# Performance work log

Hardware: AMD Instinct MI355X
Metric: run time of the kernel (lower is better)

## Reference

```python
import jax, jax.numpy as jnp
import numpy as np

B, S, H, D = 4, 8192, 8, 64  # batch, seq, heads, head_dim
M = 64                        # num random features
EPS = 1e-6


def setup_inputs() -> dict:
    key = jax.random.key(0)
    k1, k2, k3, k4 = jax.random.split(key, 4)
    qs = jax.random.normal(k1, (B, S, H, D), dtype=jnp.float32)
    ks = jax.random.normal(k2, (B, S, H, D), dtype=jnp.float32)
    vs = jax.random.normal(k3, (B, S, H, D), dtype=jnp.float32)
    proj = jax.random.normal(k4, (M, D), dtype=jnp.float32)
    return {"qs": qs, "ks": ks, "vs": vs, "proj": proj}


def _phi(x, proj):
    # stable positive softmax kernel: exp(x @ proj^T - ||x||^2/2) / sqrt(m)
    m = proj.shape[0]
    x_proj = jnp.einsum('...d,md->...m', x, proj)
    h = jnp.sum(jnp.square(x), axis=-1, keepdims=True) * 0.5
    return jnp.exp(x_proj - h) / jnp.sqrt(jnp.asarray(m, x.dtype))


def reference(qs, ks, vs, proj):
    Bq, Q, Hh, Dqk = qs.shape
    K = ks.shape[1]
    Dv = vs.shape[-1]
    # (B, S, H, D) -> (B*H, S, D)
    q = qs.transpose(0, 2, 1, 3).reshape(-1, Q, Dqk)
    k = ks.transpose(0, 2, 1, 3).reshape(-1, K, Dqk)
    v = vs.transpose(0, 2, 1, 3).reshape(-1, K, Dv)
    normalizer = 1.0 / jnp.power(jnp.asarray(Dqk, q.dtype), 0.25)
    q_prime = _phi(q * normalizer, proj)  # (B*H, Q, M)
    k_prime = _phi(k * normalizer, proj)  # (B*H, K, M)
    # fast_attend: linear-time attention
    c = jnp.concatenate([v, jnp.ones((*v.shape[:-1], 1), v.dtype)], axis=-1)  # (B*H, K, Dv+1)
    buf1 = jnp.einsum('bkm,bkc->bmc', k_prime, c)   # (B*H, M, Dv+1)
    buf2 = jnp.einsum('bqm,bmc->bqc', q_prime, buf1)  # (B*H, Q, Dv+1)
    num, den = buf2[..., :-1], buf2[..., -1]
    den = jnp.where(den < EPS, EPS, den)
    ctx = num / den[..., None]
    return ctx.reshape(Bq, Hh, Q, Dv).transpose(0, 2, 1, 3)
```

## Files before the change

### kernel.cpp

```cpp
#include <hip/hip_runtime.h>
#include <hip/hip_bf16.h>

#define S_ 8192
#define H_ 8
#define D_ 64
#define M_ 64
#define BH_ 32
#define CPK_ 80
#define NCH_ 16
#define NCHQ 16
#define TILE 64
#define QTILES (S_ / NCHQ / TILE)

typedef short bf16x8 __attribute__((ext_vector_type(8)));
typedef float f32x4 __attribute__((ext_vector_type(4)));

constexpr float XS_ = 0.35355339059327373f * 1.4426950408889634f;
constexpr float HS_ = 0.34657359027997264f;
constexpr float EPS_ = 1e-6f;

__device__ __forceinline__ unsigned short f2bf(float f) {
    unsigned int u = __float_as_uint(f);
    u += 0x7FFFu + ((u >> 16) & 1u);
    return (unsigned short)(u >> 16);
}
__device__ __forceinline__ unsigned int pkbf(float lo, float hi) {
    __hip_bfloat162 t = __float22bfloat162_rn(float2{lo, hi});
    return *reinterpret_cast<unsigned int*>(&t);
}
__device__ __forceinline__ float fexp2(float x) { return __builtin_amdgcn_exp2f(x); }

#define MFMA(a, b, c) __builtin_amdgcn_mfma_f32_16x16x32_bf16((a), (b), (c), 0, 0, 0)
#define SWZ(byteoff, row) ((byteoff) ^ (((row) & 7) << 4))

__global__ void __launch_bounds__(256, 2)
fa_k(const float* __restrict__ ks, const float* __restrict__ vs,
     const float* __restrict__ proj, float* __restrict__ partial)
{
    const int chunk = blockIdx.x;
    const int bh    = blockIdx.y;
    const int b = bh >> 3, h = bh & 7;
    const int tid = threadIdx.x, wid = tid >> 6, lane = tid & 63;
    const int l15 = lane & 15, g = lane >> 4;

    __shared__ __align__(16) char vT[4][2][64 * 64];
    __shared__ float red[M_ * CPK_];

    const size_t rs = (size_t)H_ * D_;
    const float* kb = ks + ((size_t)b * S_ * H_ + h) * D_;
    const float* vb = vs + ((size_t)b * S_ * H_ + h) * D_;
    const int rbase = chunk * 512 + wid * 128;

    bf16x8 pf[4][2];
#pragma unroll
    for (int mt = 0; mt < 4; ++mt)
#pragma unroll
        for (int kk = 0; kk < 2; ++kk) {
            const float* p = proj + (mt * 16 + l15) * D_ + kk * 32 + g * 8;
            float4 a = *(const float4*)p, c = *(const float4*)(p + 4);
            union { bf16x8 v; unsigned int u[4]; } F;
            F.u[0] = pkbf(a.x, a.y); F.u[1] = pkbf(a.z, a.w);
            F.u[2] = pkbf(c.x, c.y); F.u[3] = pkbf(c.z, c.w);
            pf[mt][kk] = F.v;
        }

    bf16x8 onef = {0, 0, 0, 0, 0, 0, 0, 0};
    if (l15 == 0) {
#pragma unroll
        for (int j = 0; j < 8; ++j) onef[j] = (short)0x3F80;
    }

    f32x4 acc[4][5];
#pragma unroll
    for (int mt = 0; mt < 4; ++mt)
#pragma unroll
        for (int ci = 0; ci < 5; ++ci) acc[mt][ci] = (f32x4){0.f, 0.f, 0.f, 0.f};

    f32x4 paE[4];
    float hrE[4];

    auto loadX = [&](int t, float4* kp, float4* vp) {
        const float* kr = kb + (size_t)(rbase + t * 16 + l15) * rs;
        kp[0] = *(const float4*)(kr + g * 8);
        kp[1] = *(const float4*)(kr + g * 8 + 4);
        kp[2] = *(const float4*)(kr + 32 + g * 8);
        kp[3] = *(const float4*)(kr + 32 + g * 8 + 4);
        const float* vr = vb + (size_t)(rbase + t * 16 + l15) * rs;
        vp[0] = *(const float4*)(vr + g * 8);
        vp[1] = *(const float4*)(vr + g * 8 + 4);
        vp[2] = *(const float4*)(vr + 32 + g * 8);
        vp[3] = *(const float4*)(vr + 32 + g * 8 + 4);
    };

    auto body = [&](int t, const float4* kc, const float4* vc,
                    float4* kn2, float4* vn2) {
        if (t + 2 < 8) loadX(t + 2, kn2, vn2);

        float kx[16];
#pragma unroll
        for (int i = 0; i < 4; ++i) {
            kx[4*i+0] = kc[i].x * XS_; kx[4*i+1] = kc[i].y * XS_;
            kx[4*i+2] = kc[i].z * XS_; kx[4*i+3] = kc[i].w * XS_;
        }
        float sq = 0.f;
#pragma unroll
        for (int j = 0; j < 16; ++j) sq += kx[j] * kx[j];
        sq += __shfl_xor(sq, 16);
        sq += __shfl_xor(sq, 32);
        float hrow = sq * HS_ + 3.0f;

        union { bf16x8 v; unsigned int u[4]; } A0, A1;
#pragma unroll
        for (int i = 0; i < 4; ++i) {
            A0.u[i] = pkbf(kx[2*i], kx[2*i+1]);
            A1.u[i] = pkbf(kx[8+2*i], kx[9+2*i]);
        }

        f32x4 pa[4];
#pragma unroll
        for (int mt = 0; mt < 4; ++mt) {
            pa[mt] = (f32x4){0.f, 0.f, 0.f, 0.f};
            pa[mt] = MFMA(A0.v, pf[mt][0], pa[mt]);
            pa[mt] = MFMA(A1.v, pf[mt][1], pa[mt]);
        }

        float hr[4];
#pragma unroll
        for (int r = 0; r < 4; ++r) hr[r] = __shfl(hrow, 4 * g + r);

        {
            char* vtp = (char*)vT + wid * 8192 + ((t >> 1) & 1) * 4096;
            int slot2 = 2 * (((l15 >> 2) & 3) * 8 + 4 * (t & 1) + (l15 & 3));
            float vv[16];
#pragma unroll
            for (int i = 0; i < 4; ++i) {
                vv[4*i+0] = vc[i].x; vv[4*i+1] = vc[i].y;
                vv[4*i+2] = vc[i].z; vv[4*i+3] = vc[i].w;
            }
#pragma unroll
            for (int p2 = 0; p2 < 4; ++p2) {
                int cA = g * 8 + 2 * p2;
                unsigned int pA = pkbf(vv[2*p2], vv[2*p2+1]);
                *(unsigned short*)(vtp + cA * 64 + (slot2 ^ ((cA & 3) << 4))) =
                    (unsigned short)pA;
                int cB = cA + 1;
                *(unsigned short*)(vtp + cB * 64 + (slot2 ^ ((cB & 3) << 4))) =
                    (unsigned short)(pA >> 16);
                int cC = 32 + cA;
                unsigned int pB = pkbf(vv[8+2*p2], vv[9+2*p2]);
                *(unsigned short*)(vtp + cC * 64 + (slot2 ^ ((cC & 3) << 4))) =
                    (unsigned short)pB;
                int cD = cC + 1;
                *(unsigned short*)(vtp + cD * 64 + (slot2 ^ ((cD & 3) << 4))) =
                    (unsigned short)(pB >> 16);
            }
        }

        if ((t & 1) == 0) {
#pragma unroll
            for (int mt = 0; mt < 4; ++mt) paE[mt] = pa[mt];
#pragma unroll
            for (int r = 0; r < 4; ++r) hrE[r] = hr[r];
        } else {
            bf16x8 eA[4];
#pragma unroll
            for (int mt = 0; mt < 4; ++mt) {
                union { bf16x8 v; unsigned int u[4]; } E;
                E.u[0] = pkbf(fexp2(paE[mt][0]-hrE[0]), fexp2(paE[mt][1]-hrE[1]));
                E.u[1] = pkbf(fexp2(paE[mt][2]-hrE[2]), fexp2(paE[mt][3]-hrE[3]));
                E.u[2] = pkbf(fexp2(pa[mt][0]-hr[0]),   fexp2(pa[mt][1]-hr[1]));
                E.u[3] = pkbf(fexp2(pa[mt][2]-hr[2]),   fexp2(pa[mt][3]-hr[3]));
                eA[mt] = E.v;
            }
            const char* vb2 = (const char*)vT + wid * 8192 + ((t >> 1) & 1) * 4096;
            bf16x8 vB[4];
#pragma unroll
            for (int ct = 0; ct < 4; ++ct) {
                int c = ct * 16 + l15;
                vB[ct] = *(const bf16x8*)(vb2 + c * 64 + ((16 * g) ^ ((c & 3) << 4)));
            }
#pragma unroll
            for (int mt = 0; mt < 4; ++mt) {
#pragma unroll
                for (int ct = 0; ct < 4; ++ct)
                    acc[mt][ct] = MFMA(eA[mt], vB[ct], acc[mt][ct]);
                acc[mt][4] = MFMA(eA[mt], onef, acc[mt][4]);
            }
        }
    };

    float4 kA[4], vA[4], kB[4], vB_[4], kC[4], vC[4];
    loadX(0, kA, vA);
    loadX(1, kB, vB_);
    body(0, kA, vA, kC, vC);
    body(1, kB, vB_, kA, vA);
    body(2, kC, vC, kB, vB_);
    body(3, kA, vA, kC, vC);
    body(4, kB, vB_, kA, vA);
    body(5, kC, vC, kB, vB_);
    body(6, kA, vA, kC, vC);
    body(7, kB, vB_, kA, vA);

    for (int i = tid; i < M_ * CPK_; i += 256) red[i] = 0.f;
    __syncthreads();
    for (int w = 0; w < 4; ++w) {
        if (wid == w) {
#pragma unroll
            for (int mt = 0; mt < 4; ++mt)
#pragma unroll
                for (int ct = 0; ct < 5; ++ct)
#pragma unroll
                    for (int r = 0; r < 4; ++r)
                        red[(mt*16 + 4*g + r) * CPK_ + ct*16 + l15] += acc[mt][ct][r];
        }
        __syncthreads();
    }
    float* dst = partial + ((size_t)bh * NCH_ + chunk) * (M_ * CPK_);
    for (int i = tid; i < M_ * CPK_; i += 256) dst[i] = red[i];
}

__global__ void __launch_bounds__(256)
fa_r(const float* __restrict__ partial, float* __restrict__ buf1, int nch)
{
    int e = blockIdx.x * 256 + threadIdx.x;
    if (e >= BH_ * M_ * CPK_) return;
    int bh = e / (M_ * CPK_);
    int r  = e - bh * (M_ * CPK_);
    const float* src = partial + (size_t)bh * nch * (M_ * CPK_) + r;
    float s0 = 0.f, s1 = 0.f, s2 = 0.f, s3 = 0.f;
    int ch = 0;
    for (; ch + 4 <= nch; ch += 4) {
        s0 += src[(size_t)(ch + 0) * (M_ * CPK_)];
        s1 += src[(size_t)(ch + 1) * (M_ * CPK_)];
        s2 += src[(size_t)(ch + 2) * (M_ * CPK_)];
        s3 += src[(size_t)(ch + 3) * (M_ * CPK_)];
    }
    for (; ch < nch; ++ch) s0 += src[(size_t)ch * (M_ * CPK_)];
    buf1[e] = (s0 + s1) + (s2 + s3);
}

__global__ void __launch_bounds__(256)
fa_q(const float* __restrict__ qs, const float* __restrict__ proj,
     const float* __restrict__ buf1, float* __restrict__ out)
{
    const int chunk = blockIdx.x;
    const int bh    = blockIdx.y;
    const int b = bh >> 3, h = bh & 7;
    const int tid = threadIdx.x, wid = tid >> 6, lane = tid & 63;
    const int l15 = lane & 15, g = lane >> 4;

    __shared__ __align__(16) char eLb[2][TILE * M_ * 2];
    __shared__ __align__(16) char b1tb[CPK_ * M_ * 2];

    const int rows = S_ / NCHQ;
    const int s0 = chunk * rows;
    const size_t rs = (size_t)H_ * D_;
    const float* qb = qs + ((size_t)b * S_ * H_ + h) * D_;

    const float* b1 = buf1 + (size_t)bh * (M_ * CPK_);
    for (int i = tid; i < M_ * CPK_; i += 256) {
        int m = i / CPK_, c = i - m * CPK_;
        *(unsigned short*)(b1tb + SWZ(c * 128 + 2 * m, c)) = f2bf(b1[i]);
    }

    bf16x8 pf[4][2];
#pragma unroll
    for (int mt = 0; mt < 4; ++mt)
#pragma unroll
        for (int kk = 0; kk < 2; ++kk) {
            const float* p = proj + (mt * 16 + l15) * D_ + kk * 32 + g * 8;
            float4 a = *(const float4*)p, c = *(const float4*)(p + 4);
            union { bf16x8 v; unsigned int u[4]; } F;
            F.u[0] = pkbf(a.x, a.y); F.u[1] = pkbf(a.z, a.w);
            F.u[2] = pkbf(c.x, c.y); F.u[3] = pkbf(c.z, c.w);
            pf[mt][kk] = F.v;
        }
    __syncthreads();

    bf16x8 af3[5][2];
#pragma unroll
    for (int ci = 0; ci < 5; ++ci)
#pragma unroll
        for (int kk = 0; kk < 2; ++kk) {
            int c = ci * 16 + l15;
            af3[ci][kk] = *(const bf16x8*)(b1tb + SWZ(c * 128 + 16 * g + 64 * kk, c));
        }

    auto loadQ = [&](int t, float4* qp) {
        int sb = s0 + t * TILE;
        const float* qrow = qb + (size_t)(sb + wid * 16 + l15) * rs;
        qp[0] = *(const float4*)(qrow + g * 8);
        qp[1] = *(const float4*)(qrow + g * 8 + 4);
        qp[2] = *(const float4*)(qrow + 32 + g * 8);
        qp[3] = *(const float4*)(qrow + 32 + g * 8 + 4);
    };

    auto body = [&](int t, int p, const float4* qc, float4* qn) {
        if (t + 1 < QTILES) loadQ(t + 1, qn);

        float kx[16];
#pragma unroll
        for (int i = 0; i < 4; ++i) {
            kx[4 * i + 0] = qc[i].x * XS_; kx[4 * i + 1] = qc[i].y * XS_;
            kx[4 * i + 2] = qc[i].z * XS_; kx[4 * i + 3] = qc[i].w * XS_;
        }
        float sq = 0.f;
#pragma unroll
        for (int j = 0; j < 16; ++j) sq += kx[j] * kx[j];
        sq += __shfl_xor(sq, 16);
        sq += __shfl_xor(sq, 32);
        float hrow = sq * HS_ + 3.0f;

        union { bf16x8 v; unsigned int u[4]; } A0, A1;
#pragma unroll
        for (int i = 0; i < 4; ++i) {
            A0.u[i] = pkbf(kx[2 * i], kx[2 * i + 1]);
            A1.u[i] = pkbf(kx[8 + 2 * i], kx[9 + 2 * i]);
        }

        f32x4 pa[4];
#pragma unroll
        for (int mt = 0; mt < 4; ++mt) {
            pa[mt] = (f32x4){0.f, 0.f, 0.f, 0.f};
            pa[mt] = MFMA(A0.v, pf[mt][0], pa[mt]);
            pa[mt] = MFMA(A1.v, pf[mt][1], pa[mt]);
        }

        float hr[4];
#pragma unroll
        for (int r = 0; r < 4; ++r) hr[r] = __shfl(hrow, 4 * g + r);

        char* elp = eLb[p];
#pragma unroll
        for (int mt = 0; mt < 4; ++mt) {
            int m = mt * 16 + l15;
            float e0 = fexp2(pa[mt][0] - hr[0]);
            float e1 = fexp2(pa[mt][1] - hr[1]);
            float e2 = fexp2(pa[mt][2] - hr[2]);
            float e3 = fexp2(pa[mt][3] - hr[3]);
            unsigned int p01 = pkbf(e0, e1), p23 = pkbf(e2, e3);
            int q0 = wid * 16 + 4 * g;
            *(unsigned short*)(elp + SWZ((q0 + 0) * 128 + 2 * m, q0 + 0)) =
                (unsigned short)p01;
            *(unsigned short*)(elp + SWZ((q0 + 1) * 128 + 2 * m, q0 + 1)) =
                (unsigned short)(p01 >> 16);
            *(unsigned short*)(elp + SWZ((q0 + 2) * 128 + 2 * m, q0 + 2)) =
                (unsigned short)p23;
            *(unsigned short*)(elp + SWZ((q0 + 3) * 128 + 2 * m, q0 + 3)) =
                (unsigned short)(p23 >> 16);
        }
        __syncthreads();

        bf16x8 b3[2];
        {
            int qrow = wid * 16 + l15;
            b3[0] = *(const bf16x8*)(elp + SWZ(qrow * 128 + 16 * g, qrow));
            b3[1] = *(const bf16x8*)(elp + SWZ(qrow * 128 + 16 * g + 64, qrow));
        }
        f32x4 dt[5];
#pragma unroll
        for (int ci = 0; ci < 5; ++ci) {
            dt[ci] = (f32x4){0.f, 0.f, 0.f, 0.f};
            dt[ci] = MFMA(af3[ci][0], b3[0], dt[ci]);
            dt[ci] = MFMA(af3[ci][1], b3[1], dt[ci]);
        }

        float den = __shfl(dt[4][0], l15);
        float rd = 1.0f / fmaxf(den, EPS_);

        int sg = s0 + t * TILE + wid * 16 + l15;
        size_t base = (((size_t)b * S_ + sg) * H_ + h) * D_;
#pragma unroll
        for (int ci = 0; ci < 4; ++ci) {
            f32x4 o;
#pragma unroll
            for (int r = 0; r < 4; ++r) o[r] = dt[ci][r] * rd;
            *(f32x4*)(out + base + ci * 16 + 4 * g) = o;
        }
    };

    float4 qa[4], qb2[4];
    loadQ(0, qa);
    for (int t = 0; t < QTILES; t += 2) {
        body(t, 0, qa, qb2);
        body(t + 1, 1, qb2, qa);
    }
}

extern "C" void kernel_launch(void* const* d_in, const int* in_sizes, int n_in,
                              void* d_out, int out_size, void* d_ws, size_t ws_size,
                              hipStream_t stream)
{
    const float* qs   = (const float*)d_in[0];
    const float* ks   = (const float*)d_in[1];
    const float* vs   = (const float*)d_in[2];
    const float* proj = (const float*)d_in[3];
    float* out = (float*)d_out;

    float* partial = (float*)d_ws;
    float* buf1 = partial + (size_t)BH_ * NCH_ * (M_ * CPK_);

    fa_k<<<dim3(NCH_, BH_), 256, 0, stream>>>(ks, vs, proj, partial);
    int nred = (BH_ * M_ * CPK_ + 255) / 256;
    fa_r<<<dim3(nred), 256, 0, stream>>>(partial, buf1, NCH_);
    fa_q<<<dim3(NCHQ, BH_), 256, 0, stream>>>(qs, proj, buf1, out);
}
```

Baseline: 74.15 us.

## Stream K/V tiles into LDS with async global_load_lds and smaller blocks

The K-feature kernel now loads K and V rows straight into a four-deep LDS ring with global_load_lds, paced by explicit vmcnt waits. This replaces the register prefetch and the manual bf16 transpose scatter of V into LDS. V is read back from the raw fp32 layout and packed to bf16 at MFMA time. Blocks shrink to two waves, the chunk count doubles to keep the grid filled, and the reduction kernel sums twice as many partials. The gain in load overlap comes with more partial traffic and more reduction work in the second kernel.

```diff
diff --git a/kernel.cpp b/kernel.cpp
--- a/kernel.cpp
+++ b/kernel.cpp
@@ -7,7 +7,7 @@
 #define M_ 64
 #define BH_ 32
 #define CPK_ 80
-#define NCH_ 16
+#define NCHK 32
 #define NCHQ 16
 #define TILE 64
 #define QTILES (S_ / NCHQ / TILE)
@@ -33,23 +33,26 @@
 #define MFMA(a, b, c) __builtin_amdgcn_mfma_f32_16x16x32_bf16((a), (b), (c), 0, 0, 0)
 #define SWZ(byteoff, row) ((byteoff) ^ (((row) & 7) << 4))
 
-__global__ void __launch_bounds__(256, 2)
+#define GLDS(src, dst) __builtin_amdgcn_global_load_lds( \
+    (const __attribute__((address_space(1))) void*)(src), \
+    (__attribute__((address_space(3))) void*)(dst), 16, 0, 0)
+
+__global__ void __launch_bounds__(128)
 fa_k(const float* __restrict__ ks, const float* __restrict__ vs,
      const float* __restrict__ proj, float* __restrict__ partial)
 {
+    __shared__ __align__(16) char pool[2][4][8192];
+
     const int chunk = blockIdx.x;
     const int bh    = blockIdx.y;
     const int b = bh >> 3, h = bh & 7;
     const int tid = threadIdx.x, wid = tid >> 6, lane = tid & 63;
     const int l15 = lane & 15, g = lane >> 4;
 
-    __shared__ __align__(16) char vT[4][2][64 * 64];
-    __shared__ float red[M_ * CPK_];
-
     const size_t rs = (size_t)H_ * D_;
     const float* kb = ks + ((size_t)b * S_ * H_ + h) * D_;
     const float* vb = vs + ((size_t)b * S_ * H_ + h) * D_;
-    const int rbase = chunk * 512 + wid * 128;
+    const int rbase = chunk * 256 + wid * 128;
 
     bf16x8 pf[4][2];
 #pragma unroll
@@ -76,31 +79,35 @@
 #pragma unroll
         for (int ci = 0; ci < 5; ++ci) acc[mt][ci] = (f32x4){0.f, 0.f, 0.f, 0.f};
 
-    f32x4 paE[4];
-    float hrE[4];
-
-    auto loadX = [&](int t, float4* kp, float4* vp) {
-        const float* kr = kb + (size_t)(rbase + t * 16 + l15) * rs;
-        kp[0] = *(const float4*)(kr + g * 8);
-        kp[1] = *(const float4*)(kr + g * 8 + 4);
-        kp[2] = *(const float4*)(kr + 32 + g * 8);
-        kp[3] = *(const float4*)(kr + 32 + g * 8 + 4);
-        const float* vr = vb + (size_t)(rbase + t * 16 + l15) * rs;
-        vp[0] = *(const float4*)(vr + g * 8);
-        vp[1] = *(const float4*)(vr + g * 8 + 4);
-        vp[2] = *(const float4*)(vr + 32 + g * 8);
-        vp[3] = *(const float4*)(vr + 32 + g * 8 + 4);
-    };
-
-    auto body = [&](int t, const float4* kc, const float4* vc,
-                    float4* kn2, float4* vn2) {
-        if (t + 2 < 8) loadX(t + 2, kn2, vn2);
-
+    auto stage = [&](int t) {
+        char* kd = pool[wid][t & 3];
+        char* vd = kd + 4096;
+        const float* krow = kb + (size_t)(rbase + t * 16 + l15) * rs;
+        const float* vrow = vb + (size_t)(rbase + t * 16 + l15) * rs;
+#pragma unroll
+        for (int i = 0; i < 4; ++i) {
+            int c0 = (i >> 1) * 32 + (i & 1) * 4 + 8 * g;
+            GLDS(krow + c0, kd + i * 1024);
+            GLDS(vrow + c0, vd + i * 1024);
+        }
+    };
+
+    f32x4 paE[4], paO[4];
+    float hrE[4], hrO[4];
+
+    auto consumeP = [&](int t, f32x4* pa, float* hr) {
+        const char* kd = pool[wid][t & 3];
+        f32x4 r0 = *(const f32x4*)(kd + lane * 16);
+        f32x4 r1 = *(const f32x4*)(kd + 1024 + lane * 16);
+        f32x4 r2 = *(const f32x4*)(kd + 2048 + lane * 16);
+        f32x4 r3 = *(const f32x4*)(kd + 3072 + lane * 16);
         float kx[16];
 #pragma unroll
-        for (int i = 0; i < 4; ++i) {
-            kx[4*i+0] = kc[i].x * XS_; kx[4*i+1] = kc[i].y * XS_;
-            kx[4*i+2] = kc[i].z * XS_; kx[4*i+3] = kc[i].w * XS_;
+        for (int j = 0; j < 4; ++j) {
+            kx[j]      = r0[j] * XS_;
+            kx[4 + j]  = r1[j] * XS_;
+            kx[8 + j]  = r2[j] * XS_;
+            kx[12 + j] = r3[j] * XS_;
         }
         float sq = 0.f;
 #pragma unroll
@@ -112,98 +119,80 @@
         union { bf16x8 v; unsigned int u[4]; } A0, A1;
 #pragma unroll
         for (int i = 0; i < 4; ++i) {
-            A0.u[i] = pkbf(kx[2*i], kx[2*i+1]);
-            A1.u[i] = pkbf(kx[8+2*i], kx[9+2*i]);
-        }
-
-        f32x4 pa[4];
+            A0.u[i] = pkbf(kx[2 * i], kx[2 * i + 1]);
+            A1.u[i] = pkbf(kx[8 + 2 * i], kx[9 + 2 * i]);
+        }
 #pragma unroll
         for (int mt = 0; mt < 4; ++mt) {
             pa[mt] = (f32x4){0.f, 0.f, 0.f, 0.f};
             pa[mt] = MFMA(A0.v, pf[mt][0], pa[mt]);
             pa[mt] = MFMA(A1.v, pf[mt][1], pa[mt]);
         }
-
-        float hr[4];
 #pragma unroll
         for (int r = 0; r < 4; ++r) hr[r] = __shfl(hrow, 4 * g + r);
-
-        {
-            char* vtp = (char*)vT + wid * 8192 + ((t >> 1) & 1) * 4096;
-            int slot2 = 2 * (((l15 >> 2) & 3) * 8 + 4 * (t & 1) + (l15 & 3));
-            float vv[16];
-#pragma unroll
-            for (int i = 0; i < 4; ++i) {
-                vv[4*i+0] = vc[i].x; vv[4*i+1] = vc[i].y;
-                vv[4*i+2] = vc[i].z; vv[4*i+3] = vc[i].w;
-            }
-#pragma unroll
-            for (int p2 = 0; p2 < 4; ++p2) {
-                int cA = g * 8 + 2 * p2;
-                unsigned int pA = pkbf(vv[2*p2], vv[2*p2+1]);
-                *(unsigned short*)(vtp + cA * 64 + (slot2 ^ ((cA & 3) << 4))) =
-                    (unsigned short)pA;
-                int cB = cA + 1;
-                *(unsigned short*)(vtp + cB * 64 + (slot2 ^ ((cB & 3) << 4))) =
-                    (unsigned short)(pA >> 16);
-                int cC = 32 + cA;
-                unsigned int pB = pkbf(vv[8+2*p2], vv[9+2*p2]);
-                *(unsigned short*)(vtp + cC * 64 + (slot2 ^ ((cC & 3) << 4))) =
-                    (unsigned short)pB;
-                int cD = cC + 1;
-                *(unsigned short*)(vtp + cD * 64 + (slot2 ^ ((cD & 3) << 4))) =
-                    (unsigned short)(pB >> 16);
-            }
-        }
-
-        if ((t & 1) == 0) {
-#pragma unroll
-            for (int mt = 0; mt < 4; ++mt) paE[mt] = pa[mt];
-#pragma unroll
-            for (int r = 0; r < 4; ++r) hrE[r] = hr[r];
-        } else {
-            bf16x8 eA[4];
-#pragma unroll
-            for (int mt = 0; mt < 4; ++mt) {
-                union { bf16x8 v; unsigned int u[4]; } E;
-                E.u[0] = pkbf(fexp2(paE[mt][0]-hrE[0]), fexp2(paE[mt][1]-hrE[1]));
-                E.u[1] = pkbf(fexp2(paE[mt][2]-hrE[2]), fexp2(paE[mt][3]-hrE[3]));
-                E.u[2] = pkbf(fexp2(pa[mt][0]-hr[0]),   fexp2(pa[mt][1]-hr[1]));
-                E.u[3] = pkbf(fexp2(pa[mt][2]-hr[2]),   fexp2(pa[mt][3]-hr[3]));
-                eA[mt] = E.v;
-            }
-            const char* vb2 = (const char*)vT + wid * 8192 + ((t >> 1) & 1) * 4096;
-            bf16x8 vB[4];
-#pragma unroll
-            for (int ct = 0; ct < 4; ++ct) {
-                int c = ct * 16 + l15;
-                vB[ct] = *(const bf16x8*)(vb2 + c * 64 + ((16 * g) ^ ((c & 3) << 4)));
-            }
-#pragma unroll
-            for (int mt = 0; mt < 4; ++mt) {
-#pragma unroll
-                for (int ct = 0; ct < 4; ++ct)
-                    acc[mt][ct] = MFMA(eA[mt], vB[ct], acc[mt][ct]);
-                acc[mt][4] = MFMA(eA[mt], onef, acc[mt][4]);
-            }
-        }
-    };
-
-    float4 kA[4], vA[4], kB[4], vB_[4], kC[4], vC[4];
-    loadX(0, kA, vA);
-    loadX(1, kB, vB_);
-    body(0, kA, vA, kC, vC);
-    body(1, kB, vB_, kA, vA);
-    body(2, kC, vC, kB, vB_);
-    body(3, kA, vA, kC, vC);
-    body(4, kB, vB_, kA, vA);
-    body(5, kC, vC, kB, vB_);
-    body(6, kA, vA, kC, vC);
-    body(7, kB, vB_, kA, vA);
-
-    for (int i = tid; i < M_ * CPK_; i += 256) red[i] = 0.f;
+    };
+
+    auto EV = [&](int t) {
+        const char* vE = pool[wid][t & 3] + 4096;
+        const char* vO = pool[wid][(t + 1) & 3] + 4096;
+        bf16x8 eA[4];
+#pragma unroll
+        for (int mt = 0; mt < 4; ++mt) {
+            union { bf16x8 v; unsigned int u[4]; } E;
+            E.u[0] = pkbf(fexp2(paE[mt][0] - hrE[0]), fexp2(paE[mt][1] - hrE[1]));
+            E.u[1] = pkbf(fexp2(paE[mt][2] - hrE[2]), fexp2(paE[mt][3] - hrE[3]));
+            E.u[2] = pkbf(fexp2(paO[mt][0] - hrO[0]), fexp2(paO[mt][1] - hrO[1]));
+            E.u[3] = pkbf(fexp2(paO[mt][2] - hrO[2]), fexp2(paO[mt][3] - hrO[3]));
+            eA[mt] = E.v;
+        }
+#pragma unroll
+        for (int ct = 0; ct < 4; ++ct) {
+            int c = ct * 16 + l15;
+            int ic = ((c >> 5) << 1) | ((c >> 2) & 1);
+            int boff = ic * 1024 + ((c & 31) >> 3) * 256 + (c & 3) * 4 + 64 * g;
+            float e0 = *(const float*)(vE + boff);
+            float e1 = *(const float*)(vE + boff + 16);
+            float e2 = *(const float*)(vE + boff + 32);
+            float e3 = *(const float*)(vE + boff + 48);
+            float o0 = *(const float*)(vO + boff);
+            float o1 = *(const float*)(vO + boff + 16);
+            float o2 = *(const float*)(vO + boff + 32);
+            float o3 = *(const float*)(vO + boff + 48);
+            union { bf16x8 v; unsigned int u[4]; } B;
+            B.u[0] = pkbf(e0, e1); B.u[1] = pkbf(e2, e3);
+            B.u[2] = pkbf(o0, o1); B.u[3] = pkbf(o2, o3);
+#pragma unroll
+            for (int mt = 0; mt < 4; ++mt)
+                acc[mt][ct] = MFMA(eA[mt], B.v, acc[mt][ct]);
+        }
+#pragma unroll
+        for (int mt = 0; mt < 4; ++mt)
+            acc[mt][4] = MFMA(eA[mt], onef, acc[mt][4]);
+    };
+
+    stage(0); stage(1); stage(2); stage(3);
+
+#define PAIR(T, W1, W2, DOSTAGE)                                   \
+    asm volatile("s_waitcnt vmcnt(" #W1 ")" ::: "memory");         \
+    __builtin_amdgcn_sched_barrier(0);                             \
+    consumeP(T, paE, hrE);                                         \
+    asm volatile("s_waitcnt vmcnt(" #W2 ")" ::: "memory");         \
+    __builtin_amdgcn_sched_barrier(0);                             \
+    consumeP(T + 1, paO, hrO);                                     \
+    EV(T);                                                         \
+    if (DOSTAGE) { stage(T + 4); stage(T + 5); }
+
+    PAIR(0, 24, 16, 1)
+    PAIR(2, 24, 16, 1)
+    PAIR(4, 24, 16, 0)
+    PAIR(6, 8, 0, 0)
+#undef PAIR
+
     __syncthreads();
-    for (int w = 0; w < 4; ++w) {
+    float* red = (float*)pool;
+    for (int i = tid; i < M_ * CPK_; i += 128) red[i] = 0.f;
+    __syncthreads();
+    for (int w = 0; w < 2; ++w) {
         if (wid == w) {
 #pragma unroll
             for (int mt = 0; mt < 4; ++mt)
@@ -211,12 +200,13 @@
                 for (int ct = 0; ct < 5; ++ct)
 #pragma unroll
                     for (int r = 0; r < 4; ++r)
-                        red[(mt*16 + 4*g + r) * CPK_ + ct*16 + l15] += acc[mt][ct][r];
+                        red[(mt * 16 + 4 * g + r) * CPK_ + ct * 16 + l15] +=
+                            acc[mt][ct][r];
         }
         __syncthreads();
     }
-    float* dst = partial + ((size_t)bh * NCH_ + chunk) * (M_ * CPK_);
-    for (int i = tid; i < M_ * CPK_; i += 256) dst[i] = red[i];
+    float* dst = partial + ((size_t)bh * NCHK + chunk) * (M_ * CPK_);
+    for (int i = tid; i < M_ * CPK_; i += 128) dst[i] = red[i];
 }
 
 __global__ void __launch_bounds__(256)
@@ -398,10 +388,10 @@
     float* out = (float*)d_out;
 
     float* partial = (float*)d_ws;
-    float* buf1 = partial + (size_t)BH_ * NCH_ * (M_ * CPK_);
-
-    fa_k<<<dim3(NCH_, BH_), 256, 0, stream>>>(ks, vs, proj, partial);
+    float* buf1 = partial + (size_t)BH_ * NCHK * (M_ * CPK_);
+
+    fa_k<<<dim3(NCHK, BH_), 128, 0, stream>>>(ks, vs, proj, partial);
     int nred = (BH_ * M_ * CPK_ + 255) / 256;
-    fa_r<<<dim3(nred), 256, 0, stream>>>(partial, buf1, NCH_);
+    fa_r<<<dim3(nred), 256, 0, stream>>>(partial, buf1, NCHK);
     fa_q<<<dim3(NCHQ, BH_), 256, 0, stream>>>(qs, proj, buf1, out);
 }
```

After: 81.70 us. +10.2%, slower.
